# Kernel tuning notes

Hardware: AMD Instinct MI355X
Metric: run time of the kernel (lower is better)

The kernel has to match this reference:

```python
import jax, jax.numpy as jnp
import numpy as np

NEG_INF = -9e15  # matches the torch module's zero_vec constant
ALPHA = 0.2      # LeakyReLU negative slope


def setup_inputs() -> dict:
    key = jax.random.key(0)
    k1, k2, k3, k4, k5, k6 = jax.random.split(key, 6)
    N_t, N_o, F_in, F_out = 8192, 8192, 256, 64
    return {
        "t_input": jax.random.normal(k1, (N_t, F_in), dtype=jnp.float32),
        "o_input": jax.random.normal(k2, (N_o, F_in), dtype=jnp.float32),
        "W_t": jax.random.normal(k3, (F_in, F_out), dtype=jnp.float32) * 0.1,
        "W_o": jax.random.normal(k4, (F_in, F_out), dtype=jnp.float32) * 0.1,
        "a": jax.random.normal(k5, (2 * F_out, 1), dtype=jnp.float32) * 0.1,
        "adj": jax.random.randint(k6, (N_t, N_o), 0, 2, dtype=jnp.int32),
    }


def reference(t_input, o_input, W_t, W_o, a, adj):
    # Linear projections
    h_t = t_input @ W_t            # [N_t, F]
    h_o = o_input @ W_o            # [N_o, F]
    F_out = h_t.shape[1]
    a_t = a[:F_out, 0]             # [F]
    a_o = a[F_out:, 0]             # [F]
    # e[i,j] = leakyrelu(cat(h_t[i], h_o[j]) . a) = leakyrelu(h_t[i].a_t + h_o[j].a_o)
    # (avoids materializing the N_t*N_o*2F concat tensor; same math)
    e = jax.nn.leaky_relu(
        (h_t @ a_t)[:, None] + (h_o @ a_o)[None, :], negative_slope=ALPHA
    )                              # [N_t, N_o]
    attention = jnp.where(adj > 0, e, NEG_INF)
    attention = jax.nn.softmax(attention, axis=1)
    # dropout is identity at eval time
    h_prime = attention @ h_o      # [N_t, F]
    return jax.nn.elu(h_prime)     # concat=True
```

## Files before the change

kernel.cpp:

```cpp
#include <hip/hip_runtime.h>
#include <math.h>

#define NT 8192
#define NO 8192
#define FIN 256
#define FOUT 64
#define SPLIT 8
#define JSP (NO/SPLIT)
#define ROWT 64
#define NW32 (NO/32)

#define OFF_ST  ((size_t)0)
#define OFF_SO  (OFF_ST + (size_t)NT)
#define OFF_WT  (OFF_SO + (size_t)NO)
#define OFF_WO  (OFF_WT + (size_t)FIN)
#define OFF_NUM (OFF_WO + (size_t)FIN)
#define OFF_DEN (OFF_NUM + (size_t)SPLIT*NT*FOUT)
#define OFF_HOB (OFF_DEN + (size_t)SPLIT*NT)
#define OFF_ETA (OFF_HOB + (size_t)NO*FOUT/2)
#define OFF_MSK (OFF_ETA + (size_t)NO*2)

typedef __attribute__((ext_vector_type(8))) short short8;
typedef __attribute__((ext_vector_type(4))) float float4v;

static __device__ __forceinline__ unsigned short f2bf(float x) {
  unsigned int u = __float_as_uint(x);
  unsigned int r = (u + 0x7fffu + ((u >> 16) & 1u)) >> 16;
  return (unsigned short)r;
}
static __device__ __forceinline__ int pk2(float a, float b) {
  return (int)((unsigned int)f2bf(a) | ((unsigned int)f2bf(b) << 16));
}
static __device__ __forceinline__ float bflo(int p) {
  return __uint_as_float(((unsigned int)p) << 16);
}
static __device__ __forceinline__ float bfhi(int p) {
  return __uint_as_float(((unsigned int)p) & 0xffff0000u);
}

__global__ void k_mask(const int* __restrict__ adj, float* __restrict__ ws) {
  unsigned int* mw = (unsigned int*)(ws + OFF_MSK);
  int wv = threadIdx.x >> 6, lane = threadIdx.x & 63;
  int gw = blockIdx.x * 4 + wv;
  const int NCH = NT*NO/256;
#pragma unroll 2
  for (int c = gw; c < NCH; c += 8192) {
    int4 a = *(const int4*)(adj + (size_t)c*256 + lane*4);
    unsigned int nib = (a.x > 0 ? 1u : 0u) | (a.y > 0 ? 2u : 0u)
                     | (a.z > 0 ? 4u : 0u) | (a.w > 0 ? 8u : 0u);
    unsigned int val = nib << ((lane & 7) * 4);
    val |= __shfl_xor((int)val, 1, 64);
    val |= __shfl_xor((int)val, 2, 64);
    val |= __shfl_xor((int)val, 4, 64);
    if ((lane & 7) == 0) mw[(size_t)c*8 + (lane >> 3)] = val;
  }
}

__global__ void k_wvec(const float* __restrict__ Wt, const float* __restrict__ Wo,
                       const float* __restrict__ a, float* __restrict__ ws) {
  int k = threadIdx.x;
  float s1 = 0.f, s2 = 0.f;
#pragma unroll
  for (int fq = 0; fq < FOUT/4; ++fq) {
    float4 wt4 = *(const float4*)(Wt + (size_t)k*FOUT + fq*4);
    float4 wo4 = *(const float4*)(Wo + (size_t)k*FOUT + fq*4);
    float4 at4 = *(const float4*)(a + fq*4);
    float4 ao4 = *(const float4*)(a + FOUT + fq*4);
    s1 += wt4.x*at4.x + wt4.y*at4.y + wt4.z*at4.z + wt4.w*at4.w;
    s2 += wo4.x*ao4.x + wo4.y*ao4.y + wo4.z*ao4.z + wo4.w*ao4.w;
  }
  ws[OFF_WT + k] = s1;
  ws[OFF_WO + k] = s2;
}

__global__ void k_st(const float* __restrict__ tin, float* __restrict__ ws) {
  int lane = threadIdx.x & 63;
  int wv   = threadIdx.x >> 6;
  int row  = blockIdx.x * 4 + wv;
  float4 v = ((const float4*)(tin + (size_t)row*FIN))[lane];
  float4 w = ((const float4*)(ws + OFF_WT))[lane];
  float p = v.x*w.x + v.y*w.y + v.z*w.z + v.w*w.w;
#pragma unroll
  for (int m = 32; m >= 1; m >>= 1) p += __shfl_xor(p, m, 64);
  if (lane == 0) ws[OFF_ST + row] = p;
}

__global__ void k_ho(const float* __restrict__ oin, const float* __restrict__ Wo,
                     const float* __restrict__ a, float* __restrict__ ws) {
  unsigned short* hobp = (unsigned short*)(ws + OFF_HOB);
  int lane = threadIdx.x & 63;
  int wv = __builtin_amdgcn_readfirstlane(threadIdx.x >> 6);
  int r0 = blockIdx.x * 16 + wv * 4;
  const float* ob = oin + (size_t)r0 * FIN;
  float acc[4];
#pragma unroll
  for (int r = 0; r < 4; ++r) acc[r] = 0.f;
#pragma unroll 2
  for (int k = 0; k < FIN; k += 4) {
    float w0 = Wo[(size_t)(k+0)*FOUT + lane];
    float w1 = Wo[(size_t)(k+1)*FOUT + lane];
    float w2 = Wo[(size_t)(k+2)*FOUT + lane];
    float w3 = Wo[(size_t)(k+3)*FOUT + lane];
#pragma unroll
    for (int r = 0; r < 4; ++r) {
      float4 ov = *(const float4*)(ob + (size_t)r*FIN + k);
      acc[r] = fmaf(ov.x, w0, acc[r]);
      acc[r] = fmaf(ov.y, w1, acc[r]);
      acc[r] = fmaf(ov.z, w2, acc[r]);
      acc[r] = fmaf(ov.w, w3, acc[r]);
    }
  }
  float ao = a[FOUT + lane];
  int fg = lane >> 4, n16 = lane & 15;
#pragma unroll
  for (int r = 0; r < 4; ++r) {
    int j = r0 + r;
    int jt = j >> 5, jl = j & 31;
    int ldst = (jl >> 3) * 16 + n16;
    int e = jl & 7;
    hobp[(((size_t)jt*4 + fg)*64 + ldst)*8 + e] = f2bf(acc[r]);
    float p = acc[r] * ao;
#pragma unroll
    for (int m = 32; m >= 1; m >>= 1) p += __shfl_xor(p, m, 64);
    if (lane == 0) ws[OFF_SO + j] = p;
  }
}

__global__ void k_etab(float* __restrict__ ws) {
  int j = blockIdx.x * 256 + threadIdx.x;
  float s = ws[OFF_SO + j];
  ws[OFF_ETA + 2*j + 0] = __expf(s);
  ws[OFF_ETA + 2*j + 1] = __expf(0.2f * s);
}

__launch_bounds__(256, 4)
__global__ void k_attn(float* __restrict__ ws) {
  const float* st = ws + OFF_ST;
  const float* etab = ws + OFF_ETA;
  const unsigned int* maskw = (const unsigned int*)(ws + OFF_MSK);
  const unsigned short* hobp = (const unsigned short*)(ws + OFF_HOB);
  float* gnum = ws + OFF_NUM;
  float* gden = ws + OFF_DEN;

  int t = threadIdx.x;
  int wv = t >> 6, lane = t & 63;
  int bx = blockIdx.x;
  int s  = bx & (SPLIT - 1);
  int bi = bx >> 3;
  int i0 = bi * ROWT;
  int jb = s * JSP;

  int rsrc = lane >> 2, csrc = lane & 3;
  int irow_s = i0 + wv*16 + rsrc;
  float sti  = st[irow_s];
  float esti  = __expf(sti);
  float esti2 = __expf(0.2f * sti);
  float ethr  = __expf(-sti);

  const unsigned int* mrow = maskw + (size_t)irow_s * NW32 + (jb >> 5);
  const float* ep = etab + (size_t)(jb + csrc*8) * 2;
  const unsigned short* hpb = hobp + (size_t)(jb >> 5) * 2048 + lane*8;

  int r16 = lane & 15, kg = lane >> 4;
  int sidx4 = ((r16 * 4 + kg) << 2);

  float4v acc0 = (float4v)0.f, acc1 = (float4v)0.f;
  float4v acc2 = (float4v)0.f, acc3 = (float4v)0.f;
  float dsum = 0.f;

#pragma unroll 1
  for (int tt = 0; tt < JSP/32; ++tt) {
    unsigned int mwv = mrow[tt];
    const float* e_ = ep + tt*64;
    float4 e0 = *(const float4*)(e_);
    float4 e1 = *(const float4*)(e_ + 4);
    float4 e2 = *(const float4*)(e_ + 8);
    float4 e3 = *(const float4*)(e_ + 12);
    const unsigned short* hb = hpb + (size_t)tt*2048;
    short8 b0 = *(const short8*)(hb);
    short8 b1 = *(const short8*)(hb + 512);
    short8 b2 = *(const short8*)(hb + 1024);
    short8 b3 = *(const short8*)(hb + 1536);

    unsigned int msh = mwv >> (csrc * 8);
    float w0 = ((e0.x >= ethr) ? esti*e0.x : esti2*e0.y); w0 = (msh & 1u)   ? w0 : 0.f;
    float w1 = ((e0.z >= ethr) ? esti*e0.z : esti2*e0.w); w1 = (msh & 2u)   ? w1 : 0.f;
    float w2 = ((e1.x >= ethr) ? esti*e1.x : esti2*e1.y); w2 = (msh & 4u)   ? w2 : 0.f;
    float w3 = ((e1.z >= ethr) ? esti*e1.z : esti2*e1.w); w3 = (msh & 8u)   ? w3 : 0.f;
    float w4 = ((e2.x >= ethr) ? esti*e2.x : esti2*e2.y); w4 = (msh & 16u)  ? w4 : 0.f;
    float w5 = ((e2.z >= ethr) ? esti*e2.z : esti2*e2.w); w5 = (msh & 32u)  ? w5 : 0.f;
    float w6 = ((e3.x >= ethr) ? esti*e3.x : esti2*e3.y); w6 = (msh & 64u)  ? w6 : 0.f;
    float w7 = ((e3.z >= ethr) ? esti*e3.z : esti2*e3.w); w7 = (msh & 128u) ? w7 : 0.f;

    int p0 = pk2(w0, w1);
    int p1 = pk2(w2, w3);
    int p2 = pk2(w4, w5);
    int p3 = pk2(w6, w7);
    dsum += bflo(p0) + bfhi(p0) + bflo(p1) + bfhi(p1)
          + bflo(p2) + bfhi(p2) + bflo(p3) + bfhi(p3);

    int4 ai;
    ai.x = __builtin_amdgcn_ds_bpermute(sidx4, p0);
    ai.y = __builtin_amdgcn_ds_bpermute(sidx4, p1);
    ai.z = __builtin_amdgcn_ds_bpermute(sidx4, p2);
    ai.w = __builtin_amdgcn_ds_bpermute(sidx4, p3);
    short8 afrag = *(short8*)&ai;

    acc0 = __builtin_amdgcn_mfma_f32_16x16x32_bf16(afrag, b0, acc0, 0, 0, 0);
    acc1 = __builtin_amdgcn_mfma_f32_16x16x32_bf16(afrag, b1, acc1, 0, 0, 0);
    acc2 = __builtin_amdgcn_mfma_f32_16x16x32_bf16(afrag, b2, acc2, 0, 0, 0);
    acc3 = __builtin_amdgcn_mfma_f32_16x16x32_bf16(afrag, b3, acc3, 0, 0, 0);
  }

  dsum += __shfl_xor(dsum, 1, 64);
  dsum += __shfl_xor(dsum, 2, 64);
  if (csrc == 0) gden[(size_t)s*NT + i0 + wv*16 + rsrc] = dsum;

  size_t obase = ((size_t)s*NT + i0 + wv*16 + kg*4) * FOUT + r16;
#pragma unroll
  for (int r = 0; r < 4; ++r) {
    gnum[obase + (size_t)r*FOUT +  0] = acc0[r];
    gnum[obase + (size_t)r*FOUT + 16] = acc1[r];
    gnum[obase + (size_t)r*FOUT + 32] = acc2[r];
    gnum[obase + (size_t)r*FOUT + 48] = acc3[r];
  }
}

__global__ void k_comb(const float* __restrict__ ws, float* __restrict__ out) {
  int idx = blockIdx.x * 256 + threadIdx.x;
  int i = idx >> 6;
  float num = 0.f, den = 0.f;
#pragma unroll
  for (int s = 0; s < SPLIT; ++s) {
    num += ws[OFF_NUM + ((size_t)s*NT + i)*FOUT + (idx & 63)];
    den += ws[OFF_DEN + (size_t)s*NT + i];
  }
  float r = num / den;
  out[idx] = (r > 0.f) ? r : (__expf(r) - 1.f);
}

extern "C" void kernel_launch(void* const* d_in, const int* in_sizes, int n_in,
                              void* d_out, int out_size, void* d_ws, size_t ws_size,
                              hipStream_t stream) {
  const float* tin = (const float*)d_in[0];
  const float* oin = (const float*)d_in[1];
  const float* Wt  = (const float*)d_in[2];
  const float* Wo  = (const float*)d_in[3];
  const float* a   = (const float*)d_in[4];
  const int*   adj = (const int*)d_in[5];
  float* out = (float*)d_out;
  float* ws  = (float*)d_ws;

  hipLaunchKernelGGL(k_mask, dim3(2048),           dim3(256), 0, stream, adj, ws);
  hipLaunchKernelGGL(k_wvec, dim3(1),              dim3(256), 0, stream, Wt, Wo, a, ws);
  hipLaunchKernelGGL(k_st,   dim3(NT/4),           dim3(256), 0, stream, tin, ws);
  hipLaunchKernelGGL(k_ho,   dim3(NO/16),          dim3(256), 0, stream, oin, Wo, a, ws);
  hipLaunchKernelGGL(k_etab, dim3(NO/256),         dim3(256), 0, stream, ws);
  hipLaunchKernelGGL(k_attn, dim3(NT/ROWT*SPLIT),  dim3(256), 0, stream, ws);
  hipLaunchKernelGGL(k_comb, dim3(NT*FOUT/256),    dim3(256), 0, stream, ws, out);
}
```

Measured before the change: 460.6 us.

## Fuse all stages into one cooperative persistent kernel with transposed mask

Replaces the seven separate launches with one cooperative kernel of 512 blocks that runs four phases separated by grid syncs, with a plain multi-launch fallback. The adjacency bitmask is now stored column-tile-major so each tile's mask words for consecutive rows sit next to each other. The precomputed exp table is dropped in favour of computing leakyrelu and exp per element inside the attention loop. SPLIT drops from 8 to 4 to match the fixed grid. The aim is to cut launch overhead and the separate passes, at the cost of more exp work in the inner loop, grid-sync costs and only 512 blocks for the attention phase.

```diff
diff --git a/kernel.cpp b/kernel.cpp
--- a/kernel.cpp
+++ b/kernel.cpp
@@ -1,14 +1,17 @@
 #include <hip/hip_runtime.h>
+#include <hip/hip_cooperative_groups.h>
 #include <math.h>
+
+namespace cg = cooperative_groups;
 
 #define NT 8192
 #define NO 8192
 #define FIN 256
 #define FOUT 64
-#define SPLIT 8
+#define SPLIT 4
 #define JSP (NO/SPLIT)
 #define ROWT 64
-#define NW32 (NO/32)
+#define NBLK 512
 
 #define OFF_ST  ((size_t)0)
 #define OFF_SO  (OFF_ST + (size_t)NT)
@@ -17,8 +20,7 @@
 #define OFF_NUM (OFF_WO + (size_t)FIN)
 #define OFF_DEN (OFF_NUM + (size_t)SPLIT*NT*FOUT)
 #define OFF_HOB (OFF_DEN + (size_t)SPLIT*NT)
-#define OFF_ETA (OFF_HOB + (size_t)NO*FOUT/2)
-#define OFF_MSK (OFF_ETA + (size_t)NO*2)
+#define OFF_MSK (OFF_HOB + (size_t)NO*FOUT/2)
 
 typedef __attribute__((ext_vector_type(8))) short short8;
 typedef __attribute__((ext_vector_type(4))) float float4v;
@@ -38,128 +40,126 @@
   return __uint_as_float(((unsigned int)p) & 0xffff0000u);
 }
 
-__global__ void k_mask(const int* __restrict__ adj, float* __restrict__ ws) {
-  unsigned int* mw = (unsigned int*)(ws + OFF_MSK);
-  int wv = threadIdx.x >> 6, lane = threadIdx.x & 63;
-  int gw = blockIdx.x * 4 + wv;
-  const int NCH = NT*NO/256;
-#pragma unroll 2
-  for (int c = gw; c < NCH; c += 8192) {
-    int4 a = *(const int4*)(adj + (size_t)c*256 + lane*4);
-    unsigned int nib = (a.x > 0 ? 1u : 0u) | (a.y > 0 ? 2u : 0u)
-                     | (a.z > 0 ? 4u : 0u) | (a.w > 0 ? 8u : 0u);
-    unsigned int val = nib << ((lane & 7) * 4);
-    val |= __shfl_xor((int)val, 1, 64);
-    val |= __shfl_xor((int)val, 2, 64);
-    val |= __shfl_xor((int)val, 4, 64);
-    if ((lane & 7) == 0) mw[(size_t)c*8 + (lane >> 3)] = val;
-  }
-}
-
-__global__ void k_wvec(const float* __restrict__ Wt, const float* __restrict__ Wo,
-                       const float* __restrict__ a, float* __restrict__ ws) {
-  int k = threadIdx.x;
+
+static __device__ __forceinline__ void phase1(const float* __restrict__ Wt,
+                                              const float* __restrict__ Wo,
+                                              const float* __restrict__ a,
+                                              float* __restrict__ ws, int t) {
   float s1 = 0.f, s2 = 0.f;
 #pragma unroll
   for (int fq = 0; fq < FOUT/4; ++fq) {
-    float4 wt4 = *(const float4*)(Wt + (size_t)k*FOUT + fq*4);
-    float4 wo4 = *(const float4*)(Wo + (size_t)k*FOUT + fq*4);
+    float4 wt4 = *(const float4*)(Wt + (size_t)t*FOUT + fq*4);
+    float4 wo4 = *(const float4*)(Wo + (size_t)t*FOUT + fq*4);
     float4 at4 = *(const float4*)(a + fq*4);
     float4 ao4 = *(const float4*)(a + FOUT + fq*4);
     s1 += wt4.x*at4.x + wt4.y*at4.y + wt4.z*at4.z + wt4.w*at4.w;
     s2 += wo4.x*ao4.x + wo4.y*ao4.y + wo4.z*ao4.z + wo4.w*ao4.w;
   }
-  ws[OFF_WT + k] = s1;
-  ws[OFF_WO + k] = s2;
-}
-
-__global__ void k_st(const float* __restrict__ tin, float* __restrict__ ws) {
-  int lane = threadIdx.x & 63;
-  int wv   = threadIdx.x >> 6;
-  int row  = blockIdx.x * 4 + wv;
-  float4 v = ((const float4*)(tin + (size_t)row*FIN))[lane];
-  float4 w = ((const float4*)(ws + OFF_WT))[lane];
-  float p = v.x*w.x + v.y*w.y + v.z*w.z + v.w*w.w;
-#pragma unroll
-  for (int m = 32; m >= 1; m >>= 1) p += __shfl_xor(p, m, 64);
-  if (lane == 0) ws[OFF_ST + row] = p;
-}
-
-__global__ void k_ho(const float* __restrict__ oin, const float* __restrict__ Wo,
-                     const float* __restrict__ a, float* __restrict__ ws) {
-  unsigned short* hobp = (unsigned short*)(ws + OFF_HOB);
-  int lane = threadIdx.x & 63;
-  int wv = __builtin_amdgcn_readfirstlane(threadIdx.x >> 6);
-  int r0 = blockIdx.x * 16 + wv * 4;
-  const float* ob = oin + (size_t)r0 * FIN;
-  float acc[4];
-#pragma unroll
-  for (int r = 0; r < 4; ++r) acc[r] = 0.f;
+  ws[OFF_WT + t] = s1;
+  ws[OFF_WO + t] = s2;
+}
+
+static __device__ __forceinline__ void phase2(const float* __restrict__ tin,
+                                              const float* __restrict__ oin,
+                                              const float* __restrict__ Wo,
+                                              const float* __restrict__ a,
+                                              const int* __restrict__ adj,
+                                              float* __restrict__ ws,
+                                              int b, int t) {
+  int wv = t >> 6, lane = t & 63;
+  {
+    float4 w = ((const float4*)(ws + OFF_WT))[lane];
+#pragma unroll
+    for (int r = 0; r < 4; ++r) {
+      int row = b*16 + wv*4 + r;
+      float4 v = ((const float4*)(tin + (size_t)row*FIN))[lane];
+      float p = v.x*w.x + v.y*w.y + v.z*w.z + v.w*w.w;
+#pragma unroll
+      for (int m = 32; m >= 1; m >>= 1) p += __shfl_xor(p, m, 64);
+      if (lane == 0) ws[OFF_ST + row] = p;
+    }
+  }
+  {
+    unsigned short* hobp = (unsigned short*)(ws + OFF_HOB);
+    int r0 = b*16 + wv*4;
+    const float* ob = oin + (size_t)r0 * FIN;
+    float acc[4];
+#pragma unroll
+    for (int r = 0; r < 4; ++r) acc[r] = 0.f;
 #pragma unroll 2
-  for (int k = 0; k < FIN; k += 4) {
-    float w0 = Wo[(size_t)(k+0)*FOUT + lane];
-    float w1 = Wo[(size_t)(k+1)*FOUT + lane];
-    float w2 = Wo[(size_t)(k+2)*FOUT + lane];
-    float w3 = Wo[(size_t)(k+3)*FOUT + lane];
+    for (int k = 0; k < FIN; k += 4) {
+      float w0 = Wo[(size_t)(k+0)*FOUT + lane];
+      float w1 = Wo[(size_t)(k+1)*FOUT + lane];
+      float w2 = Wo[(size_t)(k+2)*FOUT + lane];
+      float w3 = Wo[(size_t)(k+3)*FOUT + lane];
+#pragma unroll
+      for (int r = 0; r < 4; ++r) {
+        float4 ov = *(const float4*)(ob + (size_t)r*FIN + k);
+        acc[r] = fmaf(ov.x, w0, acc[r]);
+        acc[r] = fmaf(ov.y, w1, acc[r]);
+        acc[r] = fmaf(ov.z, w2, acc[r]);
+        acc[r] = fmaf(ov.w, w3, acc[r]);
+      }
+    }
+    float ao = a[FOUT + lane];
+    int fg = lane >> 4, n16 = lane & 15;
 #pragma unroll
     for (int r = 0; r < 4; ++r) {
-      float4 ov = *(const float4*)(ob + (size_t)r*FIN + k);
-      acc[r] = fmaf(ov.x, w0, acc[r]);
-      acc[r] = fmaf(ov.y, w1, acc[r]);
-      acc[r] = fmaf(ov.z, w2, acc[r]);
-      acc[r] = fmaf(ov.w, w3, acc[r]);
-    }
-  }
-  float ao = a[FOUT + lane];
-  int fg = lane >> 4, n16 = lane & 15;
-#pragma unroll
-  for (int r = 0; r < 4; ++r) {
-    int j = r0 + r;
-    int jt = j >> 5, jl = j & 31;
-    int ldst = (jl >> 3) * 16 + n16;
-    int e = jl & 7;
-    hobp[(((size_t)jt*4 + fg)*64 + ldst)*8 + e] = f2bf(acc[r]);
-    float p = acc[r] * ao;
-#pragma unroll
-    for (int m = 32; m >= 1; m >>= 1) p += __shfl_xor(p, m, 64);
-    if (lane == 0) ws[OFF_SO + j] = p;
-  }
-}
-
-__global__ void k_etab(float* __restrict__ ws) {
-  int j = blockIdx.x * 256 + threadIdx.x;
-  float s = ws[OFF_SO + j];
-  ws[OFF_ETA + 2*j + 0] = __expf(s);
-  ws[OFF_ETA + 2*j + 1] = __expf(0.2f * s);
-}
-
-__launch_bounds__(256, 4)
-__global__ void k_attn(float* __restrict__ ws) {
+      int j = r0 + r;
+      int jt = j >> 5, jl = j & 31;
+      int ldst = (jl >> 3) * 16 + n16;
+      int e = jl & 7;
+      hobp[(((size_t)jt*4 + fg)*64 + ldst)*8 + e] = f2bf(acc[r]);
+      float p = acc[r] * ao;
+#pragma unroll
+      for (int m = 32; m >= 1; m >>= 1) p += __shfl_xor(p, m, 64);
+      if (lane == 0) ws[OFF_SO + j] = p;
+    }
+  }
+  {
+    unsigned int* mw = (unsigned int*)(ws + OFF_MSK);
+    int g = b*4 + wv;
+    int i8 = g >> 1;
+    int jw0 = (g & 1) * 128;
+    int rr = i8*8 + (lane >> 3);
+    int cc = (lane & 7) * 4;
+    const int* ar = adj + (size_t)rr*NO + cc;
+#pragma unroll 4
+    for (int pp = 0; pp < 128; ++pp) {
+      int jw = jw0 + pp;
+      int4 a4 = *(const int4*)(ar + jw*32);
+      unsigned int nib = (a4.x > 0 ? 1u : 0u) | (a4.y > 0 ? 2u : 0u)
+                       | (a4.z > 0 ? 4u : 0u) | (a4.w > 0 ? 8u : 0u);
+      unsigned int val = nib << ((lane & 7) * 4);
+      val |= __shfl_xor((int)val, 1, 64);
+      val |= __shfl_xor((int)val, 2, 64);
+      val |= __shfl_xor((int)val, 4, 64);
+      if ((lane & 7) == 0) mw[(size_t)jw*NT + i8*8 + (lane >> 3)] = val;
+    }
+  }
+}
+
+static __device__ __forceinline__ void phase3(float* __restrict__ ws, int b, int t) {
   const float* st = ws + OFF_ST;
-  const float* etab = ws + OFF_ETA;
-  const unsigned int* maskw = (const unsigned int*)(ws + OFF_MSK);
+  const float* so = ws + OFF_SO;
+  const unsigned int* mT = (const unsigned int*)(ws + OFF_MSK);
   const unsigned short* hobp = (const unsigned short*)(ws + OFF_HOB);
   float* gnum = ws + OFF_NUM;
   float* gden = ws + OFF_DEN;
 
-  int t = threadIdx.x;
   int wv = t >> 6, lane = t & 63;
-  int bx = blockIdx.x;
-  int s  = bx & (SPLIT - 1);
-  int bi = bx >> 3;
+  int s  = b & (SPLIT - 1);
+  int bi = b >> 2;
   int i0 = bi * ROWT;
   int jb = s * JSP;
 
   int rsrc = lane >> 2, csrc = lane & 3;
   int irow_s = i0 + wv*16 + rsrc;
-  float sti  = st[irow_s];
-  float esti  = __expf(sti);
-  float esti2 = __expf(0.2f * sti);
-  float ethr  = __expf(-sti);
-
-  const unsigned int* mrow = maskw + (size_t)irow_s * NW32 + (jb >> 5);
-  const float* ep = etab + (size_t)(jb + csrc*8) * 2;
-  const unsigned short* hpb = hobp + (size_t)(jb >> 5) * 2048 + lane*8;
+  float sti = st[irow_s];
+
+  const unsigned int* mrow = mT + (size_t)(jb >> 5)*NT + irow_s;
+  const float* sop = so + jb + csrc*8;
+  const unsigned short* hpb = hobp + (size_t)(jb >> 5)*2048 + lane*8;
 
   int r16 = lane & 15, kg = lane >> 4;
   int sidx4 = ((r16 * 4 + kg) << 2);
@@ -170,12 +170,9 @@
 
 #pragma unroll 1
   for (int tt = 0; tt < JSP/32; ++tt) {
-    unsigned int mwv = mrow[tt];
-    const float* e_ = ep + tt*64;
-    float4 e0 = *(const float4*)(e_);
-    float4 e1 = *(const float4*)(e_ + 4);
-    float4 e2 = *(const float4*)(e_ + 8);
-    float4 e3 = *(const float4*)(e_ + 12);
+    unsigned int mwv = mrow[(size_t)tt*NT];
+    float4 s0 = *(const float4*)(sop + tt*32);
+    float4 s1 = *(const float4*)(sop + tt*32 + 4);
     const unsigned short* hb = hpb + (size_t)tt*2048;
     short8 b0 = *(const short8*)(hb);
     short8 b1 = *(const short8*)(hb + 512);
@@ -183,14 +180,22 @@
     short8 b3 = *(const short8*)(hb + 1536);
 
     unsigned int msh = mwv >> (csrc * 8);
-    float w0 = ((e0.x >= ethr) ? esti*e0.x : esti2*e0.y); w0 = (msh & 1u)   ? w0 : 0.f;
-    float w1 = ((e0.z >= ethr) ? esti*e0.z : esti2*e0.w); w1 = (msh & 2u)   ? w1 : 0.f;
-    float w2 = ((e1.x >= ethr) ? esti*e1.x : esti2*e1.y); w2 = (msh & 4u)   ? w2 : 0.f;
-    float w3 = ((e1.z >= ethr) ? esti*e1.z : esti2*e1.w); w3 = (msh & 8u)   ? w3 : 0.f;
-    float w4 = ((e2.x >= ethr) ? esti*e2.x : esti2*e2.y); w4 = (msh & 16u)  ? w4 : 0.f;
-    float w5 = ((e2.z >= ethr) ? esti*e2.z : esti2*e2.w); w5 = (msh & 32u)  ? w5 : 0.f;
-    float w6 = ((e3.x >= ethr) ? esti*e3.x : esti2*e3.y); w6 = (msh & 64u)  ? w6 : 0.f;
-    float w7 = ((e3.z >= ethr) ? esti*e3.z : esti2*e3.w); w7 = (msh & 128u) ? w7 : 0.f;
+    float x0 = sti + s0.x; x0 = fmaxf(x0, 0.2f*x0);
+    float x1 = sti + s0.y; x1 = fmaxf(x1, 0.2f*x1);
+    float x2 = sti + s0.z; x2 = fmaxf(x2, 0.2f*x2);
+    float x3 = sti + s0.w; x3 = fmaxf(x3, 0.2f*x3);
+    float x4 = sti + s1.x; x4 = fmaxf(x4, 0.2f*x4);
+    float x5 = sti + s1.y; x5 = fmaxf(x5, 0.2f*x5);
+    float x6 = sti + s1.z; x6 = fmaxf(x6, 0.2f*x6);
+    float x7 = sti + s1.w; x7 = fmaxf(x7, 0.2f*x7);
+    float w0 = (msh & 1u)   ? __expf(x0) : 0.f;
+    float w1 = (msh & 2u)   ? __expf(x1) : 0.f;
+    float w2 = (msh & 4u)   ? __expf(x2) : 0.f;
+    float w3 = (msh & 8u)   ? __expf(x3) : 0.f;
+    float w4 = (msh & 16u)  ? __expf(x4) : 0.f;
+    float w5 = (msh & 32u)  ? __expf(x5) : 0.f;
+    float w6 = (msh & 64u)  ? __expf(x6) : 0.f;
+    float w7 = (msh & 128u) ? __expf(x7) : 0.f;
 
     int p0 = pk2(w0, w1);
     int p1 = pk2(w2, w3);
@@ -226,17 +231,57 @@
   }
 }
 
-__global__ void k_comb(const float* __restrict__ ws, float* __restrict__ out) {
-  int idx = blockIdx.x * 256 + threadIdx.x;
-  int i = idx >> 6;
-  float num = 0.f, den = 0.f;
-#pragma unroll
-  for (int s = 0; s < SPLIT; ++s) {
-    num += ws[OFF_NUM + ((size_t)s*NT + i)*FOUT + (idx & 63)];
-    den += ws[OFF_DEN + (size_t)s*NT + i];
-  }
-  float r = num / den;
-  out[idx] = (r > 0.f) ? r : (__expf(r) - 1.f);
+static __device__ __forceinline__ void phase4(const float* __restrict__ ws,
+                                              float* __restrict__ out, int b, int t) {
+#pragma unroll
+  for (int q = 0; q < 4; ++q) {
+    int idx = b*1024 + q*256 + t;
+    int i = idx >> 6;
+    float num = 0.f, den = 0.f;
+#pragma unroll
+    for (int s = 0; s < SPLIT; ++s) {
+      num += ws[OFF_NUM + ((size_t)s*NT + i)*FOUT + (idx & 63)];
+      den += ws[OFF_DEN + (size_t)s*NT + i];
+    }
+    float r = num / den;
+    out[idx] = (r > 0.f) ? r : (__expf(r) - 1.f);
+  }
+}
+
+__launch_bounds__(256, 2)
+__global__ void k_fused(const float* __restrict__ tin, const float* __restrict__ oin,
+                        const float* __restrict__ Wt, const float* __restrict__ Wo,
+                        const float* __restrict__ a, const int* __restrict__ adj,
+                        float* __restrict__ ws, float* __restrict__ out) {
+  cg::grid_group grid = cg::this_grid();
+  int t = threadIdx.x, b = blockIdx.x;
+  if (b == 0) phase1(Wt, Wo, a, ws, t);
+  grid.sync();
+  phase2(tin, oin, Wo, a, adj, ws, b, t);
+  grid.sync();
+  phase3(ws, b, t);
+  grid.sync();
+  phase4(ws, out, b, t);
+}
+
+__launch_bounds__(256, 2)
+__global__ void k_p1(const float* __restrict__ Wt, const float* __restrict__ Wo,
+                     const float* __restrict__ a, float* __restrict__ ws) {
+  phase1(Wt, Wo, a, ws, threadIdx.x);
+}
+__launch_bounds__(256, 2)
+__global__ void k_p2(const float* __restrict__ tin, const float* __restrict__ oin,
+                     const float* __restrict__ Wo, const float* __restrict__ a,
+                     const int* __restrict__ adj, float* __restrict__ ws) {
+  phase2(tin, oin, Wo, a, adj, ws, blockIdx.x, threadIdx.x);
+}
+__launch_bounds__(256, 2)
+__global__ void k_p3(float* __restrict__ ws) {
+  phase3(ws, blockIdx.x, threadIdx.x);
+}
+__launch_bounds__(256, 2)
+__global__ void k_p4(const float* __restrict__ ws, float* __restrict__ out) {
+  phase4(ws, out, blockIdx.x, threadIdx.x);
 }
 
 extern "C" void kernel_launch(void* const* d_in, const int* in_sizes, int n_in,
@@ -251,11 +296,21 @@
   float* out = (float*)d_out;
   float* ws  = (float*)d_ws;
 
-  hipLaunchKernelGGL(k_mask, dim3(2048),           dim3(256), 0, stream, adj, ws);
-  hipLaunchKernelGGL(k_wvec, dim3(1),              dim3(256), 0, stream, Wt, Wo, a, ws);
-  hipLaunchKernelGGL(k_st,   dim3(NT/4),           dim3(256), 0, stream, tin, ws);
-  hipLaunchKernelGGL(k_ho,   dim3(NO/16),          dim3(256), 0, stream, oin, Wo, a, ws);
-  hipLaunchKernelGGL(k_etab, dim3(NO/256),         dim3(256), 0, stream, ws);
-  hipLaunchKernelGGL(k_attn, dim3(NT/ROWT*SPLIT),  dim3(256), 0, stream, ws);
-  hipLaunchKernelGGL(k_comb, dim3(NT*FOUT/256),    dim3(256), 0, stream, ws, out);
-}
+  int nb = 0;
+  hipError_t qe = hipOccupancyMaxActiveBlocksPerMultiprocessor(
+      &nb, (const void*)k_fused, 256, 0);
+  bool coop_ok = (qe == hipSuccess) && (nb >= 2);
+
+  if (coop_ok) {
+    void* args[] = {(void*)&tin, (void*)&oin, (void*)&Wt, (void*)&Wo,
+                    (void*)&a, (void*)&adj, (void*)&ws, (void*)&out};
+    hipError_t le = hipLaunchCooperativeKernel((const void*)k_fused,
+                                               dim3(NBLK), dim3(256),
+                                               args, 0, stream);
+    if (le == hipSuccess) return;
+  }
+  hipLaunchKernelGGL(k_p1, dim3(1),    dim3(256), 0, stream, Wt, Wo, a, ws);
+  hipLaunchKernelGGL(k_p2, dim3(NBLK), dim3(256), 0, stream, tin, oin, Wo, a, adj, ws);
+  hipLaunchKernelGGL(k_p3, dim3(NBLK), dim3(256), 0, stream, ws);
+  hipLaunchKernelGGL(k_p4, dim3(NBLK), dim3(256), 0, stream, ws, out);
+}
```

New measurement: 657.3 us. 42.7% more time.
